# Performance work log

Measured on AMD Instinct MI355X. Metric: run time of the kernel, lower is better.

Reference implementation:

```python
import jax, jax.numpy as jnp
import numpy as np

N = 100000   # nodes
F = 128      # input features
H = 128      # hidden = 2*output_dim
Z = 64       # output_dim
E = 1600000  # message-passing edges
EP = 200000  # pos/neg decode edges each


def setup_inputs() -> dict:
    key = jax.random.key(0)
    ks = jax.random.split(key, 6)
    x = jax.random.normal(ks[0], (N, F), dtype=jnp.float32)
    edge_index = jax.random.randint(ks[1], (2, E), 0, N, dtype=jnp.int64)
    pos_edge = jax.random.randint(ks[2], (2, EP), 0, N, dtype=jnp.int64)
    neg_edge = jax.random.randint(ks[3], (2, EP), 0, N, dtype=jnp.int64)
    W1 = jax.random.normal(ks[4], (F, H), dtype=jnp.float32) / np.float32(np.sqrt(F))
    b1 = jnp.zeros((H,), jnp.float32)
    W2 = jax.random.normal(ks[5], (H, Z), dtype=jnp.float32) / np.float32(np.sqrt(H))
    b2 = jnp.zeros((Z,), jnp.float32)
    return dict(x=x, W1=W1, b1=b1, W2=W2, b2=b2,
                edge_index=edge_index, pos_edge=pos_edge, neg_edge=neg_edge)


def _gcn_conv(x, src, dst, norm, W, b, n):
    # x' = scatter_add_dst(norm * (x @ W)[src]) + b   (GCNConv, sym-normalized, self-loops)
    h = x @ W                         # [N, out]
    msg = h[src] * norm[:, None]      # [E+N, out] gather + scale
    out = jax.ops.segment_sum(msg, dst, num_segments=n)
    return out + b


def reference(x, W1, b1, W2, b2, edge_index, pos_edge, neg_edge):
    # add self-loops (GCNConv default)
    loop = jnp.arange(N, dtype=edge_index.dtype)
    src = jnp.concatenate([edge_index[0], loop])
    dst = jnp.concatenate([edge_index[1], loop])
    # symmetric normalization deg^-1/2[src] * deg^-1/2[dst]
    deg = jax.ops.segment_sum(jnp.ones(dst.shape, x.dtype), dst, num_segments=N)
    dinv = jnp.where(deg > 0, jax.lax.rsqrt(deg), 0.0)
    norm = dinv[src] * dinv[dst]
    # encoder: GCN -> ReLU -> GCN
    h = jax.nn.relu(_gcn_conv(x, src, dst, norm, W1, b1, N))
    latent = _gcn_conv(h, src, dst, norm, W2, b2, N)
    # decoder: edge dot products on pos+neg edges
    e = jnp.concatenate([pos_edge, neg_edge], axis=-1)  # [2, 2*EP]
    logits = jnp.sum(latent[e[0]] * latent[e[1]], axis=-1)
    return logits
```

## Files before the change

kernel.cpp:

```cpp
#include <hip/hip_runtime.h>

#define N_NODES 100000
#define F_IN    128
#define H_DIM   128
#define Z_DIM   64
#define E_EDGES 1600000
#define EP_EDGES 200000

#define BSHIFT 7
#define NBUCK  ((N_NODES + 127) >> 7)
#define CHUNK  4096
#define NCHUNK ((E_EDGES + CHUNK - 1) / CHUNK)

typedef __attribute__((ext_vector_type(8))) short short8;
typedef __attribute__((ext_vector_type(4))) float f32x4;
typedef unsigned int uint;
typedef unsigned short ushort;

__device__ __forceinline__ ushort f2bf(float f) {
    uint u = __float_as_uint(f);
    u += 0x7fffu + ((u >> 16) & 1u);
    return (ushort)(u >> 16);
}
__device__ __forceinline__ float bflo(uint u) { return __uint_as_float(u << 16); }
__device__ __forceinline__ float bfhi(uint u) { return __uint_as_float(u & 0xffff0000u); }


__global__ __launch_bounds__(256) void zero_gcur_kernel(int* __restrict__ gcur) {
    int i = blockIdx.x * 256 + threadIdx.x;
    if (i < 1024) gcur[i] = 0;
}


__global__ __launch_bounds__(256) void bhist_kernel(const int* __restrict__ dst,
                                                    int* __restrict__ ghist) {
    __shared__ int lh[NBUCK];
    for (int i = threadIdx.x; i < NBUCK; i += 256) lh[i] = 0;
    __syncthreads();
    int base = blockIdx.x * CHUNK;
    int end = min(base + CHUNK, E_EDGES);
    for (int e = base + threadIdx.x; e < end; e += 256)
        atomicAdd(&lh[dst[e] >> BSHIFT], 1);
    __syncthreads();
    for (int i = threadIdx.x; i < NBUCK; i += 256)
        if (lh[i]) atomicAdd(&ghist[i], lh[i]);
}


__global__ __launch_bounds__(1024) void bscan_kernel(int* __restrict__ gc) {
    __shared__ int s[1024];
    int t = threadIdx.x;
    int v = (t < NBUCK) ? gc[t] : 0;
    s[t] = v;
    __syncthreads();
    #pragma unroll
    for (int off = 1; off < 1024; off <<= 1) {
        int x = (t >= off) ? s[t - off] : 0;
        __syncthreads();
        s[t] += x;
        __syncthreads();
    }
    if (t < NBUCK) gc[t] = s[t] - v;
}


__global__ __launch_bounds__(256) void bscatter_kernel(const int* __restrict__ src,
                                                       const int* __restrict__ dst,
                                                       int* __restrict__ gcursor,
                                                       int2* __restrict__ sorted) {
    __shared__ int lh[NBUCK];
    __shared__ int lbase[NBUCK];
    for (int i = threadIdx.x; i < NBUCK; i += 256) lh[i] = 0;
    __syncthreads();
    int base = blockIdx.x * CHUNK;
    int end = min(base + CHUNK, E_EDGES);
    for (int e = base + threadIdx.x; e < end; e += 256)
        atomicAdd(&lh[dst[e] >> BSHIFT], 1);
    __syncthreads();
    for (int i = threadIdx.x; i < NBUCK; i += 256)
        lbase[i] = lh[i] ? atomicAdd(&gcursor[i], lh[i]) : 0;
    __syncthreads();
    for (int e = base + threadIdx.x; e < end; e += 256) {
        int d = dst[e];
        int p = atomicAdd(&lbase[d >> BSHIFT], 1);
        sorted[p] = make_int2(src[e], d);
    }
}


__global__ __launch_bounds__(256) void bucket_csr_kernel(const int2* __restrict__ sorted,
                                                         const int* __restrict__ gcur,
                                                         int* __restrict__ csr,
                                                         int* __restrict__ ends,
                                                         float* __restrict__ dinv) {
    __shared__ int lcnt[128], lcur[128];
    int b = blockIdx.x, t = threadIdx.x;
    int bstart = b ? gcur[b - 1] : 0;
    int bend = gcur[b];
    if (t < 128) lcnt[t] = 0;
    __syncthreads();
    for (int i = bstart + t; i < bend; i += 256)
        atomicAdd(&lcnt[sorted[i].y & 127], 1);
    __syncthreads();
    if (t < 64) {
        int c0 = lcnt[t], c1 = lcnt[t + 64];
        int s0 = c0;
        #pragma unroll
        for (int d = 1; d < 64; d <<= 1) {
            int x = __shfl_up(s0, d, 64);
            if (t >= d) s0 += x;
        }
        int tot0 = __shfl(s0, 63, 64);
        int s1 = c1;
        #pragma unroll
        for (int d = 1; d < 64; d <<= 1) {
            int x = __shfl_up(s1, d, 64);
            if (t >= d) s1 += x;
        }
        s1 += tot0;
        lcur[t] = s0 - c0;
        lcur[t + 64] = s1 - c1;
        int n0 = b * 128 + t, n1 = n0 + 64;
        if (n0 < N_NODES) { ends[n0] = bstart + s0; dinv[n0] = rsqrtf(1.0f + (float)c0); }
        if (n1 < N_NODES) { ends[n1] = bstart + s1; dinv[n1] = rsqrtf(1.0f + (float)c1); }
    }
    __syncthreads();
    for (int i = bstart + t; i < bend; i += 256) {
        int2 sd = sorted[i];
        int p = bstart + atomicAdd(&lcur[sd.y & 127], 1);
        csr[p] = sd.x;
    }
}


__global__ __launch_bounds__(256) void wprep_kernel(const float* __restrict__ W1,
                                                    const float* __restrict__ W2,
                                                    ushort* __restrict__ W1T,
                                                    ushort* __restrict__ W2T) {
    int i = blockIdx.x * 256 + threadIdx.x;
    if (i < 128 * 128) {
        int n = i >> 7, k = i & 127;
        W1T[i] = f2bf(W1[k * 128 + n]);
    }
    int j = i - 128 * 128;
    if (j >= 0 && j < 64 * 128) {
        int n = j >> 7, k = j & 127;
        W2T[j] = f2bf(W2[k * 64 + n]);
    }
}


template<int NC, bool A_F32>
__global__ __launch_bounds__(256) void gemm_mfma_kernel(const void* __restrict__ Ap,
                                                        const ushort* __restrict__ BT,
                                                        const float* __restrict__ dinv,
                                                        ushort* __restrict__ C, int M) {
    constexpr int NT = NC / 16;
    __shared__ ushort Bs[4 * NT * 64 * 8];

    for (int idx = threadIdx.x; idx < 4 * NT * 64; idx += 256) {
        int l   = idx & 63;
        int nt  = (idx >> 6) % NT;
        int kc  = idx / (64 * NT);
        int m16 = l & 15, quad = l >> 4;
        ((short8*)Bs)[idx] =
            *(const short8*)(BT + ((nt * 16 + m16) * 128 + kc * 32 + quad * 8));
    }
    __syncthreads();

    int wave = threadIdx.x >> 6, lane = threadIdx.x & 63;
    int m16 = lane & 15, quad = lane >> 4;
    int row0 = (blockIdx.x * 4 + wave) * 16;
    if (row0 >= M) return;
    int arow = row0 + m16;
    if (arow >= M) arow = M - 1;

    f32x4 acc[NT];
    #pragma unroll
    for (int t = 0; t < NT; ++t) acc[t] = (f32x4){0.f, 0.f, 0.f, 0.f};

    #pragma unroll
    for (int kc = 0; kc < 4; ++kc) {
        short8 a;
        if (A_F32) {
            const float* A = (const float*)Ap;
            const float4* p = (const float4*)(A + (size_t)arow * 128 + kc * 32 + quad * 8);
            float4 x0 = p[0], x1 = p[1];
            a[0] = (short)f2bf(x0.x); a[1] = (short)f2bf(x0.y);
            a[2] = (short)f2bf(x0.z); a[3] = (short)f2bf(x0.w);
            a[4] = (short)f2bf(x1.x); a[5] = (short)f2bf(x1.y);
            a[6] = (short)f2bf(x1.z); a[7] = (short)f2bf(x1.w);
        } else {
            a = *(const short8*)((const ushort*)Ap + (size_t)arow * 128 + kc * 32 + quad * 8);
        }
        #pragma unroll
        for (int nt = 0; nt < NT; ++nt) {
            short8 b = ((const short8*)Bs)[(kc * NT + nt) * 64 + lane];
            acc[nt] = __builtin_amdgcn_mfma_f32_16x16x32_bf16(a, b, acc[nt], 0, 0, 0);
        }
    }

    #pragma unroll
    for (int r = 0; r < 4; ++r) {
        int row = row0 + quad * 4 + r;
        if (row < M) {
            float dr = dinv[row];
            #pragma unroll
            for (int nt = 0; nt < NT; ++nt)
                C[(size_t)row * NC + nt * 16 + m16] = f2bf(acc[nt][r] * dr);
        }
    }
}


__global__ __launch_bounds__(256) void gather128_kernel(const ushort* __restrict__ feat,
                                                        const float* __restrict__ bias,
                                                        const float* __restrict__ dinv,
                                                        const int* __restrict__ ends,
                                                        const int* __restrict__ csr,
                                                        ushort* __restrict__ out) {
    int wave = threadIdx.x >> 6, lane = threadIdx.x & 63;
    int half = lane >> 5, sl = lane & 31;
    int n = blockIdx.x * 4 + wave;
    const uint2* fu = (const uint2*)feat;

    float a0 = 0.f, a1 = 0.f, a2 = 0.f, a3 = 0.f;
    if (half == 0) {
        uint2 s = fu[(size_t)n * 32 + sl];
        a0 = bflo(s.x); a1 = bfhi(s.x); a2 = bflo(s.y); a3 = bfhi(s.y);
    }
    int j0 = n ? ends[n - 1] : 0, j1 = ends[n];
    int j = j0 + half;
    for (; j + 6 < j1; j += 8) {
        int s0 = csr[j], s1 = csr[j + 2], s2 = csr[j + 4], s3 = csr[j + 6];
        uint2 f0 = fu[(size_t)s0 * 32 + sl];
        uint2 f1 = fu[(size_t)s1 * 32 + sl];
        uint2 f2 = fu[(size_t)s2 * 32 + sl];
        uint2 f3 = fu[(size_t)s3 * 32 + sl];
        a0 += bflo(f0.x) + bflo(f1.x) + bflo(f2.x) + bflo(f3.x);
        a1 += bfhi(f0.x) + bfhi(f1.x) + bfhi(f2.x) + bfhi(f3.x);
        a2 += bflo(f0.y) + bflo(f1.y) + bflo(f2.y) + bflo(f3.y);
        a3 += bfhi(f0.y) + bfhi(f1.y) + bfhi(f2.y) + bfhi(f3.y);
    }
    for (; j < j1; j += 2) {
        uint2 f = fu[(size_t)csr[j] * 32 + sl];
        a0 += bflo(f.x); a1 += bfhi(f.x); a2 += bflo(f.y); a3 += bfhi(f.y);
    }
    a0 += __shfl_xor(a0, 32, 64);
    a1 += __shfl_xor(a1, 32, 64);
    a2 += __shfl_xor(a2, 32, 64);
    a3 += __shfl_xor(a3, 32, 64);
    if (half == 0) {
        float dn = dinv[n];
        float r0 = fmaxf(bias[sl * 4 + 0] + dn * a0, 0.f);
        float r1 = fmaxf(bias[sl * 4 + 1] + dn * a1, 0.f);
        float r2 = fmaxf(bias[sl * 4 + 2] + dn * a2, 0.f);
        float r3 = fmaxf(bias[sl * 4 + 3] + dn * a3, 0.f);
        uint2 o;
        o.x = (uint)f2bf(r0) | ((uint)f2bf(r1) << 16);
        o.y = (uint)f2bf(r2) | ((uint)f2bf(r3) << 16);
        ((uint2*)out)[(size_t)n * 32 + sl] = o;
    }
}


__global__ __launch_bounds__(256) void gather64_kernel(const ushort* __restrict__ feat,
                                                       const float* __restrict__ bias,
                                                       const float* __restrict__ dinv,
                                                       const int* __restrict__ ends,
                                                       const int* __restrict__ csr,
                                                       float* __restrict__ out) {
    int wave = threadIdx.x >> 6, lane = threadIdx.x & 63;
    int half = lane >> 5, sl = lane & 31;
    int n = blockIdx.x * 4 + wave;
    const uint* fu = (const uint*)feat;

    float a0 = 0.f, a1 = 0.f;
    if (half == 0) {
        uint s = fu[(size_t)n * 32 + sl];
        a0 = bflo(s); a1 = bfhi(s);
    }
    int j0 = n ? ends[n - 1] : 0, j1 = ends[n];
    int j = j0 + half;
    for (; j + 6 < j1; j += 8) {
        int s0 = csr[j], s1 = csr[j + 2], s2 = csr[j + 4], s3 = csr[j + 6];
        uint f0 = fu[(size_t)s0 * 32 + sl];
        uint f1 = fu[(size_t)s1 * 32 + sl];
        uint f2 = fu[(size_t)s2 * 32 + sl];
        uint f3 = fu[(size_t)s3 * 32 + sl];
        a0 += bflo(f0) + bflo(f1) + bflo(f2) + bflo(f3);
        a1 += bfhi(f0) + bfhi(f1) + bfhi(f2) + bfhi(f3);
    }
    for (; j < j1; j += 2) {
        uint f = fu[(size_t)csr[j] * 32 + sl];
        a0 += bflo(f); a1 += bfhi(f);
    }
    a0 += __shfl_xor(a0, 32, 64);
    a1 += __shfl_xor(a1, 32, 64);
    if (half == 0) {
        float dn = dinv[n];
        float2 o;
        o.x = bias[sl * 2]     + dn * a0;
        o.y = bias[sl * 2 + 1] + dn * a1;
        ((float2*)out)[(size_t)n * 32 + sl] = o;
    }
}


__global__ __launch_bounds__(256) void decode_kernel(const float* __restrict__ latent,
                                                     const int* __restrict__ pos,
                                                     const int* __restrict__ neg,
                                                     float* __restrict__ out) {
    int gwave = (blockIdx.x * 256 + threadIdx.x) >> 6;
    int lane = threadIdx.x & 63;
    int e0 = gwave * 4;
    if (e0 >= 2 * EP_EDGES) return;

    int ia[4], ib[4];
    #pragma unroll
    for (int u = 0; u < 4; ++u) {
        int edge = e0 + u;
        if (edge < EP_EDGES) {
            ia[u] = pos[edge];
            ib[u] = pos[EP_EDGES + edge];
        } else {
            int e2 = edge - EP_EDGES;
            ia[u] = neg[e2];
            ib[u] = neg[EP_EDGES + e2];
        }
    }
    float v[4];
    #pragma unroll
    for (int u = 0; u < 4; ++u)
        v[u] = latent[(size_t)ia[u] * Z_DIM + lane] * latent[(size_t)ib[u] * Z_DIM + lane];
    #pragma unroll
    for (int u = 0; u < 4; ++u) {
        float s = v[u];
        #pragma unroll
        for (int off = 32; off > 0; off >>= 1) s += __shfl_down(s, off, 64);
        if (lane == 0) out[e0 + u] = s;
    }
}


extern "C" void kernel_launch(void* const* d_in, const int* in_sizes, int n_in,
                              void* d_out, int out_size, void* d_ws, size_t ws_size,
                              hipStream_t stream) {
    const float* x  = (const float*)d_in[0];
    const float* W1 = (const float*)d_in[1];
    const float* b1 = (const float*)d_in[2];
    const float* W2 = (const float*)d_in[3];
    const float* b2 = (const float*)d_in[4];
    const int* edge_index = (const int*)d_in[5];
    const int* pos = (const int*)d_in[6];
    const int* neg = (const int*)d_in[7];
    float* out = (float*)d_out;

    const int* src = edge_index;
    const int* dst = edge_index + E_EDGES;

    float*  dinv   = (float*)d_ws;
    int*    ends   = (int*)(dinv + N_NODES);
    int*    gcur   = ends + N_NODES;
    int2*   sorted = (int2*)(gcur + 1024);
    int*    csr    = (int*)(sorted + E_EDGES);
    ushort* W1T    = (ushort*)(csr + E_EDGES);
    ushort* W2T    = W1T + 128 * 128;
    ushort* bufH   = W2T + 64 * 128;
    ushort* bufR   = bufH + (size_t)N_NODES * 128;

    zero_gcur_kernel<<<4, 256, 0, stream>>>(gcur);
    bhist_kernel<<<NCHUNK, 256, 0, stream>>>(dst, gcur);
    bscan_kernel<<<1, 1024, 0, stream>>>(gcur);
    bscatter_kernel<<<NCHUNK, 256, 0, stream>>>(src, dst, gcur, sorted);
    bucket_csr_kernel<<<NBUCK, 256, 0, stream>>>(sorted, gcur, csr, ends, dinv);

    wprep_kernel<<<96, 256, 0, stream>>>(W1, W2, W1T, W2T);

    const int GEMM_GRID = (N_NODES + 63) / 64;

    gemm_mfma_kernel<128, true><<<GEMM_GRID, 256, 0, stream>>>(x, W1T, dinv, bufH, N_NODES);

    gather128_kernel<<<N_NODES / 4, 256, 0, stream>>>(bufH, b1, dinv, ends, csr, bufR);

    gemm_mfma_kernel<64, false><<<GEMM_GRID, 256, 0, stream>>>(bufR, W2T, dinv, bufH, N_NODES);

    float* latent = (float*)bufR;
    gather64_kernel<<<N_NODES / 4, 256, 0, stream>>>(bufH, b2, dinv, ends, csr, latent);

    decode_kernel<<<(2 * EP_EDGES) / 16, 256, 0, stream>>>(latent, pos, neg, out);
}
```

Baseline: 345.8 us.

## Split gathers into feature-half passes and pack sorted edges into one int

The gather kernels now run two passes over feature halves (grid doubled), so each pass touches half the feature table and may fit better in L2/MALL during random neighbor gathers. The 64-wide gather uses quarter-wave lanes with 16 lanes per row. The bucket sort also packs src and the low dst bits into a single int instead of an int2, halving sorted-buffer traffic. In exchange the CSR indices and ends are read twice and gather rows become narrower 64/128-byte accesses.

```diff
diff --git a/kernel.cpp b/kernel.cpp
--- a/kernel.cpp
+++ b/kernel.cpp
@@ -11,6 +11,7 @@
 #define NBUCK  ((N_NODES + 127) >> 7)
 #define CHUNK  4096
 #define NCHUNK ((E_EDGES + CHUNK - 1) / CHUNK)
+#define GBLK   (N_NODES / 4)
 
 typedef __attribute__((ext_vector_type(8))) short short8;
 typedef __attribute__((ext_vector_type(4))) float f32x4;
@@ -67,7 +68,7 @@
 __global__ __launch_bounds__(256) void bscatter_kernel(const int* __restrict__ src,
                                                        const int* __restrict__ dst,
                                                        int* __restrict__ gcursor,
-                                                       int2* __restrict__ sorted) {
+                                                       int* __restrict__ sorted) {
     __shared__ int lh[NBUCK];
     __shared__ int lbase[NBUCK];
     for (int i = threadIdx.x; i < NBUCK; i += 256) lh[i] = 0;
@@ -83,12 +84,12 @@
     for (int e = base + threadIdx.x; e < end; e += 256) {
         int d = dst[e];
         int p = atomicAdd(&lbase[d >> BSHIFT], 1);
-        sorted[p] = make_int2(src[e], d);
-    }
-}
-
-
-__global__ __launch_bounds__(256) void bucket_csr_kernel(const int2* __restrict__ sorted,
+        sorted[p] = (src[e] << 7) | (d & 127);
+    }
+}
+
+
+__global__ __launch_bounds__(256) void bucket_csr_kernel(const int* __restrict__ sorted,
                                                          const int* __restrict__ gcur,
                                                          int* __restrict__ csr,
                                                          int* __restrict__ ends,
@@ -100,7 +101,7 @@
     if (t < 128) lcnt[t] = 0;
     __syncthreads();
     for (int i = bstart + t; i < bend; i += 256)
-        atomicAdd(&lcnt[sorted[i].y & 127], 1);
+        atomicAdd(&lcnt[sorted[i] & 127], 1);
     __syncthreads();
     if (t < 64) {
         int c0 = lcnt[t], c1 = lcnt[t + 64];
@@ -126,9 +127,9 @@
     }
     __syncthreads();
     for (int i = bstart + t; i < bend; i += 256) {
-        int2 sd = sorted[i];
-        int p = bstart + atomicAdd(&lcur[sd.y & 127], 1);
-        csr[p] = sd.x;
+        int v = sorted[i];
+        int p = bstart + atomicAdd(&lcur[v & 127], 1);
+        csr[p] = v >> 7;
     }
 }
 
@@ -213,96 +214,93 @@
 }
 
 
-__global__ __launch_bounds__(256) void gather128_kernel(const ushort* __restrict__ feat,
+__global__ __launch_bounds__(256) void gather128h_kernel(const ushort* __restrict__ feat,
+                                                         const float* __restrict__ bias,
+                                                         const float* __restrict__ dinv,
+                                                         const int* __restrict__ ends,
+                                                         const int* __restrict__ csr,
+                                                         ushort* __restrict__ out) {
+    int wave = threadIdx.x >> 6, lane = threadIdx.x & 63;
+    int half = lane >> 5, sl = lane & 31;
+    int pass = blockIdx.x / GBLK;
+    int nb   = blockIdx.x - pass * GBLK;
+    int n = nb * 4 + wave;
+    const uint* fu = (const uint*)feat;
+    size_t hoff = (size_t)pass * 32;
+
+    float a0 = 0.f, a1 = 0.f;
+    if (half == 0) {
+        uint s = fu[(size_t)n * 64 + hoff + sl];
+        a0 = bflo(s); a1 = bfhi(s);
+    }
+    int j0 = n ? ends[n - 1] : 0, j1 = ends[n];
+    int j = j0 + half;
+    for (; j + 6 < j1; j += 8) {
+        int s0 = csr[j], s1 = csr[j + 2], s2 = csr[j + 4], s3 = csr[j + 6];
+        uint f0 = fu[(size_t)s0 * 64 + hoff + sl];
+        uint f1 = fu[(size_t)s1 * 64 + hoff + sl];
+        uint f2 = fu[(size_t)s2 * 64 + hoff + sl];
+        uint f3 = fu[(size_t)s3 * 64 + hoff + sl];
+        a0 += bflo(f0) + bflo(f1) + bflo(f2) + bflo(f3);
+        a1 += bfhi(f0) + bfhi(f1) + bfhi(f2) + bfhi(f3);
+    }
+    for (; j < j1; j += 2) {
+        uint f = fu[(size_t)csr[j] * 64 + hoff + sl];
+        a0 += bflo(f); a1 += bfhi(f);
+    }
+    a0 += __shfl_xor(a0, 32, 64);
+    a1 += __shfl_xor(a1, 32, 64);
+    if (half == 0) {
+        float dn = dinv[n];
+        int f = pass * 64 + sl * 2;
+        float r0 = fmaxf(bias[f]     + dn * a0, 0.f);
+        float r1 = fmaxf(bias[f + 1] + dn * a1, 0.f);
+        ((uint*)out)[(size_t)n * 64 + hoff + sl] = (uint)f2bf(r0) | ((uint)f2bf(r1) << 16);
+    }
+}
+
+
+__global__ __launch_bounds__(256) void gather64h_kernel(const ushort* __restrict__ feat,
                                                         const float* __restrict__ bias,
                                                         const float* __restrict__ dinv,
                                                         const int* __restrict__ ends,
                                                         const int* __restrict__ csr,
-                                                        ushort* __restrict__ out) {
+                                                        float* __restrict__ out) {
     int wave = threadIdx.x >> 6, lane = threadIdx.x & 63;
-    int half = lane >> 5, sl = lane & 31;
-    int n = blockIdx.x * 4 + wave;
-    const uint2* fu = (const uint2*)feat;
-
-    float a0 = 0.f, a1 = 0.f, a2 = 0.f, a3 = 0.f;
-    if (half == 0) {
-        uint2 s = fu[(size_t)n * 32 + sl];
-        a0 = bflo(s.x); a1 = bfhi(s.x); a2 = bflo(s.y); a3 = bfhi(s.y);
+    int q = lane >> 4, sl = lane & 15;
+    int pass = blockIdx.x / GBLK;
+    int nb   = blockIdx.x - pass * GBLK;
+    int n = nb * 4 + wave;
+    const uint* fu = (const uint*)feat;
+    size_t hoff = (size_t)pass * 16;
+
+    float a0 = 0.f, a1 = 0.f;
+    if (q == 0) {
+        uint s = fu[(size_t)n * 32 + hoff + sl];
+        a0 = bflo(s); a1 = bfhi(s);
     }
     int j0 = n ? ends[n - 1] : 0, j1 = ends[n];
-    int j = j0 + half;
-    for (; j + 6 < j1; j += 8) {
-        int s0 = csr[j], s1 = csr[j + 2], s2 = csr[j + 4], s3 = csr[j + 6];
-        uint2 f0 = fu[(size_t)s0 * 32 + sl];
-        uint2 f1 = fu[(size_t)s1 * 32 + sl];
-        uint2 f2 = fu[(size_t)s2 * 32 + sl];
-        uint2 f3 = fu[(size_t)s3 * 32 + sl];
-        a0 += bflo(f0.x) + bflo(f1.x) + bflo(f2.x) + bflo(f3.x);
-        a1 += bfhi(f0.x) + bfhi(f1.x) + bfhi(f2.x) + bfhi(f3.x);
-        a2 += bflo(f0.y) + bflo(f1.y) + bflo(f2.y) + bflo(f3.y);
-        a3 += bfhi(f0.y) + bfhi(f1.y) + bfhi(f2.y) + bfhi(f3.y);
-    }
-    for (; j < j1; j += 2) {
-        uint2 f = fu[(size_t)csr[j] * 32 + sl];
-        a0 += bflo(f.x); a1 += bfhi(f.x); a2 += bflo(f.y); a3 += bfhi(f.y);
-    }
-    a0 += __shfl_xor(a0, 32, 64);
-    a1 += __shfl_xor(a1, 32, 64);
-    a2 += __shfl_xor(a2, 32, 64);
-    a3 += __shfl_xor(a3, 32, 64);
-    if (half == 0) {
+    int j = j0 + q;
+    for (; j + 4 < j1; j += 8) {
+        int s0 = csr[j], s1 = csr[j + 4];
+        uint f0 = fu[(size_t)s0 * 32 + hoff + sl];
+        uint f1 = fu[(size_t)s1 * 32 + hoff + sl];
+        a0 += bflo(f0) + bflo(f1);
+        a1 += bfhi(f0) + bfhi(f1);
+    }
+    for (; j < j1; j += 4) {
+        uint f = fu[(size_t)csr[j] * 32 + hoff + sl];
+        a0 += bflo(f); a1 += bfhi(f);
+    }
+    a0 += __shfl_xor(a0, 16, 64); a0 += __shfl_xor(a0, 32, 64);
+    a1 += __shfl_xor(a1, 16, 64); a1 += __shfl_xor(a1, 32, 64);
+    if (q == 0) {
         float dn = dinv[n];
-        float r0 = fmaxf(bias[sl * 4 + 0] + dn * a0, 0.f);
-        float r1 = fmaxf(bias[sl * 4 + 1] + dn * a1, 0.f);
-        float r2 = fmaxf(bias[sl * 4 + 2] + dn * a2, 0.f);
-        float r3 = fmaxf(bias[sl * 4 + 3] + dn * a3, 0.f);
-        uint2 o;
-        o.x = (uint)f2bf(r0) | ((uint)f2bf(r1) << 16);
-        o.y = (uint)f2bf(r2) | ((uint)f2bf(r3) << 16);
-        ((uint2*)out)[(size_t)n * 32 + sl] = o;
-    }
-}
-
-
-__global__ __launch_bounds__(256) void gather64_kernel(const ushort* __restrict__ feat,
-                                                       const float* __restrict__ bias,
-                                                       const float* __restrict__ dinv,
-                                                       const int* __restrict__ ends,
-                                                       const int* __restrict__ csr,
-                                                       float* __restrict__ out) {
-    int wave = threadIdx.x >> 6, lane = threadIdx.x & 63;
-    int half = lane >> 5, sl = lane & 31;
-    int n = blockIdx.x * 4 + wave;
-    const uint* fu = (const uint*)feat;
-
-    float a0 = 0.f, a1 = 0.f;
-    if (half == 0) {
-        uint s = fu[(size_t)n * 32 + sl];
-        a0 = bflo(s); a1 = bfhi(s);
-    }
-    int j0 = n ? ends[n - 1] : 0, j1 = ends[n];
-    int j = j0 + half;
-    for (; j + 6 < j1; j += 8) {
-        int s0 = csr[j], s1 = csr[j + 2], s2 = csr[j + 4], s3 = csr[j + 6];
-        uint f0 = fu[(size_t)s0 * 32 + sl];
-        uint f1 = fu[(size_t)s1 * 32 + sl];
-        uint f2 = fu[(size_t)s2 * 32 + sl];
-        uint f3 = fu[(size_t)s3 * 32 + sl];
-        a0 += bflo(f0) + bflo(f1) + bflo(f2) + bflo(f3);
-        a1 += bfhi(f0) + bfhi(f1) + bfhi(f2) + bfhi(f3);
-    }
-    for (; j < j1; j += 2) {
-        uint f = fu[(size_t)csr[j] * 32 + sl];
-        a0 += bflo(f); a1 += bfhi(f);
-    }
-    a0 += __shfl_xor(a0, 32, 64);
-    a1 += __shfl_xor(a1, 32, 64);
-    if (half == 0) {
-        float dn = dinv[n];
+        int f = pass * 32 + sl * 2;
         float2 o;
-        o.x = bias[sl * 2]     + dn * a0;
-        o.y = bias[sl * 2 + 1] + dn * a1;
-        ((float2*)out)[(size_t)n * 32 + sl] = o;
+        o.x = bias[f]     + dn * a0;
+        o.y = bias[f + 1] + dn * a1;
+        ((float2*)out)[(size_t)n * 32 + hoff + sl] = o;
     }
 }
 
@@ -362,8 +360,8 @@
     float*  dinv   = (float*)d_ws;
     int*    ends   = (int*)(dinv + N_NODES);
     int*    gcur   = ends + N_NODES;
-    int2*   sorted = (int2*)(gcur + 1024);
-    int*    csr    = (int*)(sorted + E_EDGES);
+    int*    sorted = gcur + 1024;
+    int*    csr    = sorted + E_EDGES;
     ushort* W1T    = (ushort*)(csr + E_EDGES);
     ushort* W2T    = W1T + 128 * 128;
     ushort* bufH   = W2T + 64 * 128;
@@ -381,12 +379,12 @@
 
     gemm_mfma_kernel<128, true><<<GEMM_GRID, 256, 0, stream>>>(x, W1T, dinv, bufH, N_NODES);
 
-    gather128_kernel<<<N_NODES / 4, 256, 0, stream>>>(bufH, b1, dinv, ends, csr, bufR);
+    gather128h_kernel<<<2 * GBLK, 256, 0, stream>>>(bufH, b1, dinv, ends, csr, bufR);
 
     gemm_mfma_kernel<64, false><<<GEMM_GRID, 256, 0, stream>>>(bufR, W2T, dinv, bufH, N_NODES);
 
     float* latent = (float*)bufR;
-    gather64_kernel<<<N_NODES / 4, 256, 0, stream>>>(bufH, b2, dinv, ends, csr, latent);
+    gather64h_kernel<<<2 * GBLK, 256, 0, stream>>>(bufH, b2, dinv, ends, csr, latent);
 
     decode_kernel<<<(2 * EP_EDGES) / 16, 256, 0, stream>>>(latent, pos, neg, out);
 }
```

Result: slower. 421.2 us (+21.8%).
